# Optimization experiments

Measured on AMD Instinct MI355X. Metric: run time of the kernel, lower is better.

## Reference

```python
import jax, jax.numpy as jnp
import numpy as np

# ---- config mirrored from FullyFusedNGP.__init__ (scale=1) ----
SCALE = 1.0
L, F, LOG2_T, N_MIN = 16, 2, 19, 16
T = 1 << LOG2_T  # 524288 entries per level
B = float(np.exp(np.log(2048.0 * SCALE / N_MIN) / (L - 1)))  # per_level_scale
RES = np.array([int(np.ceil(N_MIN * B**l - 1.0)) + 1 for l in range(L)], dtype=np.int32)
PRIMES = np.array([1, 2654435761, 805459861], dtype=np.uint32)  # tcnn hash primes
CORNERS = np.array([[(i >> k) & 1 for k in range(3)] for i in range(8)], dtype=np.int32)  # [8,3]
N_PTS = 262144


def hash_encode(xn, table):
    """Multi-resolution hash grid with trilinear interpolation.
    xn: [N,3] in [0,1]; table: [L,T,F] -> returns [N, L*F]."""
    res = jnp.asarray(RES)
    corners = jnp.asarray(CORNERS)
    pos = xn[None] * (res[:, None, None] - 1).astype(xn.dtype)        # [L,N,3]
    p0 = jnp.floor(pos).astype(jnp.int32)
    w = pos - p0                                                      # [L,N,3] trilinear fracs
    idx = p0[:, :, None, :] + corners[None, None]                     # [L,N,8,3]
    idx = jnp.clip(idx, 0, (res - 1)[:, None, None, None])
    ui = idx.astype(jnp.uint32)
    h = (ui[..., 0] * PRIMES[0]) ^ (ui[..., 1] * PRIMES[1]) ^ (ui[..., 2] * PRIMES[2])
    h = (h & jnp.uint32(T - 1)).astype(jnp.int32)                     # [L,N,8]
    feats = jax.vmap(lambda t, hh: t[hh])(table, h)                   # [L,N,8,F] gather
    cw = jnp.where(corners[None, None].astype(bool),
                   w[:, :, None, :], 1.0 - w[:, :, None, :]).prod(-1)  # [L,N,8]
    feat = (feats * cw[..., None]).sum(2)                             # [L,N,F]
    return jnp.moveaxis(feat, 0, 1).reshape(xn.shape[0], L * F)       # [N,32]


def sh_encode(d01):
    """Spherical harmonics degree 4 (tcnn convention, input in [0,1]). [N,3]->[N,16]."""
    d = 2.0 * d01 - 1.0
    x, y, z = d[:, 0], d[:, 1], d[:, 2]
    xy, xz, yz = x * y, x * z, y * z
    x2, y2, z2 = x * x, y * y, z * z
    return jnp.stack([
        jnp.full_like(x, 0.28209479177387814),
        -0.48860251190291987 * y,
        0.48860251190291987 * z,
        -0.48860251190291987 * x,
        1.0925484305920792 * xy,
        -1.0925484305920792 * yz,
        0.94617469575755997 * z2 - 0.31539156525251999,
        -1.0925484305920792 * xz,
        0.54627421529603959 * (x2 - y2),
        0.59004358992664352 * y * (-3.0 * x2 + y2),
        2.8906114426405538 * xy * z,
        0.45704579946446572 * y * (1.0 - 5.0 * z2),
        0.3731763325901154 * z * (5.0 * z2 - 3.0),
        0.45704579946446572 * x * (1.0 - 5.0 * z2),
        1.4453057213202769 * z * (x2 - y2),
        0.59004358992664352 * x * (-x2 + 3.0 * y2),
    ], axis=1)


def setup_inputs() -> dict:
    key = jax.random.key(0)
    ks = jax.random.split(key, 8)
    x = jax.random.uniform(ks[0], (N_PTS, 3), jnp.float32, -SCALE, SCALE)
    d = jax.random.normal(ks[1], (N_PTS, 3), jnp.float32)
    d = d / jnp.linalg.norm(d, axis=1, keepdims=True)
    table = jax.random.uniform(ks[2], (L, T, F), jnp.float32, -1e-4, 1e-4)
    def w(k, fi, fo):  # bias-free FullyFusedMLP weights
        return jax.random.normal(k, (fi, fo), jnp.float32) * (1.0 / np.sqrt(fi))
    return {
        'x': x, 'd': d, 'table': table,
        'w1': w(ks[3], 32, 64), 'w2': w(ks[4], 64, 16),
        'w_in': w(ks[5], 32, 64), 'w_h': w(ks[6], 64, 64), 'w_out': w(ks[7], 64, 3),
    }


def reference(x, d, table, w1, w2, w_in, w_h, w_out):
    xn = (x + SCALE) / (2.0 * SCALE)                 # (x - xyz_min)/(xyz_max - xyz_min)
    enc = hash_encode(xn, table)                     # [N,32]
    h = jax.nn.relu(enc @ w1) @ w2                   # density MLP, 1 hidden layer -> [N,16]
    sigmas = jnp.exp(h[:, 0])                        # TruncExp forward == exp
    sh = sh_encode((d + 1.0) * 0.5)                  # [N,16]
    a = jax.nn.relu(jnp.concatenate([sh, h], axis=1) @ w_in)
    a = jax.nn.relu(a @ w_h)
    rgbs = jax.nn.sigmoid(a @ w_out)                 # [N,3]
    return sigmas, rgbs
```

## Files before the change

### kernel.cpp

```cpp
#include <hip/hip_runtime.h>
#include <hip/hip_bf16.h>
#include <stdint.h>

typedef __bf16 bf16x8 __attribute__((ext_vector_type(8)));
typedef float  f32x4  __attribute__((ext_vector_type(4)));

__device__ __forceinline__ int imin(int a, int b) { return a < b ? a : b; }
__device__ __forceinline__ int imax(int a, int b) { return a > b ? a : b; }

#define TMASK ((1u << 19) - 1u)

__constant__ int cRES[16] = {16, 23, 31, 43, 59, 81, 112, 154,
                             213, 295, 407, 562, 777, 1073, 1483, 2048};

__global__ void __launch_bounds__(256) ngp_encode2(
    const float* __restrict__ xin,
    const float2* __restrict__ tab,
    float2* __restrict__ enc,
    int n, int nblk_half)
{
    const int bid = blockIdx.x;
    const int half = (bid >= nblk_half) ? 1 : 0;
    const int b = bid - half * nblk_half;
    const int l = (b & 7) + 8 * half;
    const int pbase = (b >> 3) * 512 + threadIdx.x;

    const int rm = cRES[l] - 1;
    const float rf = (float)rm;
    const uint32_t base = (uint32_t)l << 19;

    uint32_t idx[2][8];
    float wa[2][3];

    #pragma unroll
    for (int q = 0; q < 2; ++q) {
        const int p = pbase + q * 256;
        const float xn0 = (xin[3 * p + 0] + 1.0f) * 0.5f;
        const float xn1 = (xin[3 * p + 1] + 1.0f) * 0.5f;
        const float xn2 = (xin[3 * p + 2] + 1.0f) * 0.5f;

        const float p0 = xn0 * rf, p1 = xn1 * rf, p2 = xn2 * rf;
        const float f0 = floorf(p0), f1 = floorf(p1), f2 = floorf(p2);
        const int i0 = (int)f0, i1 = (int)f1, i2 = (int)f2;
        wa[q][0] = p0 - f0; wa[q][1] = p1 - f1; wa[q][2] = p2 - f2;

        const int a0 = imax(imin(i0, rm), 0), b0 = imax(imin(i0 + 1, rm), 0);
        const int a1 = imax(imin(i1, rm), 0), b1 = imax(imin(i1 + 1, rm), 0);
        const int a2 = imax(imin(i2, rm), 0), b2 = imax(imin(i2 + 1, rm), 0);

        const uint32_t t0a = (uint32_t)a0;
        const uint32_t t0b = (uint32_t)b0;
        const uint32_t t1a = (uint32_t)a1 * 2654435761u;
        const uint32_t t1b = (uint32_t)b1 * 2654435761u;
        const uint32_t t2a = (uint32_t)a2 * 805459861u;
        const uint32_t t2b = (uint32_t)b2 * 805459861u;

        idx[q][0] = base + ((t0a ^ t1a ^ t2a) & TMASK);
        idx[q][1] = base + ((t0b ^ t1a ^ t2a) & TMASK);
        idx[q][2] = base + ((t0a ^ t1b ^ t2a) & TMASK);
        idx[q][3] = base + ((t0b ^ t1b ^ t2a) & TMASK);
        idx[q][4] = base + ((t0a ^ t1a ^ t2b) & TMASK);
        idx[q][5] = base + ((t0b ^ t1a ^ t2b) & TMASK);
        idx[q][6] = base + ((t0a ^ t1b ^ t2b) & TMASK);
        idx[q][7] = base + ((t0b ^ t1b ^ t2b) & TMASK);
    }

    float2 v[2][8];
    #pragma unroll
    for (int q = 0; q < 2; ++q)
        #pragma unroll
        for (int cor = 0; cor < 8; ++cor)
            v[q][cor] = tab[idx[q][cor]];

    __builtin_amdgcn_sched_barrier(0);

    #pragma unroll
    for (int q = 0; q < 2; ++q) {
        const float w0 = wa[q][0], w1 = wa[q][1], w2 = wa[q][2];
        const float u0 = 1.0f - w0, u1 = 1.0f - w1, u2 = 1.0f - w2;
        float e0 = 0.0f, e1 = 0.0f;
        {   float cw = u0 * u1 * u2;  e0 = fmaf(v[q][0].x, cw, e0); e1 = fmaf(v[q][0].y, cw, e1); }
        {   float cw = w0 * u1 * u2;  e0 = fmaf(v[q][1].x, cw, e0); e1 = fmaf(v[q][1].y, cw, e1); }
        {   float cw = u0 * w1 * u2;  e0 = fmaf(v[q][2].x, cw, e0); e1 = fmaf(v[q][2].y, cw, e1); }
        {   float cw = w0 * w1 * u2;  e0 = fmaf(v[q][3].x, cw, e0); e1 = fmaf(v[q][3].y, cw, e1); }
        {   float cw = u0 * u1 * w2;  e0 = fmaf(v[q][4].x, cw, e0); e1 = fmaf(v[q][4].y, cw, e1); }
        {   float cw = w0 * u1 * w2;  e0 = fmaf(v[q][5].x, cw, e0); e1 = fmaf(v[q][5].y, cw, e1); }
        {   float cw = u0 * w1 * w2;  e0 = fmaf(v[q][6].x, cw, e0); e1 = fmaf(v[q][6].y, cw, e1); }
        {   float cw = w0 * w1 * w2;  e0 = fmaf(v[q][7].x, cw, e0); e1 = fmaf(v[q][7].y, cw, e1); }

        union { double d; float2 f; } u;
        u.f = make_float2(e0, e1);
        const int p = pbase + q * 256;
        __builtin_nontemporal_store(u.d, (double*)&enc[(size_t)l * n + p]);
    }
}

__global__ void __launch_bounds__(256) ngp_mlp_mfma(
    const float2* __restrict__ enc,
    const float* __restrict__ din,
    const float* __restrict__ W1,
    const float* __restrict__ W2,
    const float* __restrict__ WIN,
    const float* __restrict__ WH,
    const float* __restrict__ WOUT,
    float* __restrict__ out,
    int n, int ntiles)
{
    __shared__ float lds[4][16 * 68];
    const int tid  = threadIdx.x;
    const int wid  = tid >> 6;
    const int lane = tid & 63;
    const int c = lane & 15;
    const int g = lane >> 4;
    float* buf = &lds[wid][0];

    bf16x8 w1f[4], w2f[2], winf[4], whf[2][4], woutf[2];
    #pragma unroll
    for (int n4 = 0; n4 < 4; ++n4)
        #pragma unroll
        for (int j = 0; j < 8; ++j)
            w1f[n4][j] = (__bf16)W1[(g * 8 + j) * 64 + n4 * 16 + c];
    #pragma unroll
    for (int kc = 0; kc < 2; ++kc)
        #pragma unroll
        for (int j = 0; j < 8; ++j)
            w2f[kc][j] = (__bf16)W2[(kc * 32 + g * 8 + j) * 16 + c];
    #pragma unroll
    for (int n4 = 0; n4 < 4; ++n4)
        #pragma unroll
        for (int j = 0; j < 8; ++j)
            winf[n4][j] = (__bf16)WIN[(g * 8 + j) * 64 + n4 * 16 + c];
    #pragma unroll
    for (int kc = 0; kc < 2; ++kc)
        #pragma unroll
        for (int n4 = 0; n4 < 4; ++n4)
            #pragma unroll
            for (int j = 0; j < 8; ++j)
                whf[kc][n4][j] = (__bf16)WH[(kc * 32 + g * 8 + j) * 64 + n4 * 16 + c];
    #pragma unroll
    for (int kc = 0; kc < 2; ++kc)
        #pragma unroll
        for (int j = 0; j < 8; ++j)
            woutf[kc][j] = (c < 3) ? (__bf16)WOUT[(kc * 32 + g * 8 + j) * 3 + c]
                                   : (__bf16)0.0f;

    for (int t = blockIdx.x; t < ntiles; t += gridDim.x) {
        const int pbase = t * 64 + wid * 16;
        const int pc = pbase + c;

        bf16x8 a1;
        #pragma unroll
        for (int m = 0; m < 4; ++m) {
            const float2 e = enc[(size_t)(4 * g + m) * n + pc];
            a1[2 * m]     = (__bf16)e.x;
            a1[2 * m + 1] = (__bf16)e.y;
        }

        #pragma unroll
        for (int n4 = 0; n4 < 4; ++n4) {
            f32x4 d = {0.f, 0.f, 0.f, 0.f};
            d = __builtin_amdgcn_mfma_f32_16x16x32_bf16(a1, w1f[n4], d, 0, 0, 0);
            #pragma unroll
            for (int r = 0; r < 4; ++r)
                buf[(g * 4 + r) * 68 + n4 * 16 + c] = fmaxf(d[r], 0.0f);
        }

        f32x4 hacc = {0.f, 0.f, 0.f, 0.f};
        #pragma unroll
        for (int kc = 0; kc < 2; ++kc) {
            bf16x8 a2;
            const float* src = &buf[c * 68 + kc * 32 + g * 8];
            #pragma unroll
            for (int j = 0; j < 8; ++j) a2[j] = (__bf16)src[j];
            hacc = __builtin_amdgcn_mfma_f32_16x16x32_bf16(a2, w2f[kc], hacc, 0, 0, 0);
        }

        if (c == 0) {
            #pragma unroll
            for (int r = 0; r < 4; ++r)
                out[pbase + g * 4 + r] = __expf(hacc[r]);
        }

        #pragma unroll
        for (int r = 0; r < 4; ++r)
            buf[(g * 4 + r) * 68 + c] = hacc[r];

        const float dx = din[3 * pc + 0];
        const float dy = din[3 * pc + 1];
        const float dz = din[3 * pc + 2];
        const float xy = dx * dy, xz = dx * dz, yz = dy * dz;
        const float x2 = dx * dx, y2 = dy * dy, z2 = dz * dz;
        float shv[16];
        shv[0]  = 0.28209479177387814f;
        shv[1]  = -0.48860251190291987f * dy;
        shv[2]  = 0.48860251190291987f * dz;
        shv[3]  = -0.48860251190291987f * dx;
        shv[4]  = 1.0925484305920792f * xy;
        shv[5]  = -1.0925484305920792f * yz;
        shv[6]  = 0.94617469575756f * z2 - 0.31539156525252f;
        shv[7]  = -1.0925484305920792f * xz;
        shv[8]  = 0.5462742152960396f * (x2 - y2);
        shv[9]  = 0.5900435899266435f * dy * (-3.0f * x2 + y2);
        shv[10] = 2.890611442640554f * xy * dz;
        shv[11] = 0.4570457994644657f * dy * (1.0f - 5.0f * z2);
        shv[12] = 0.3731763325901154f * dz * (5.0f * z2 - 3.0f);
        shv[13] = 0.4570457994644657f * dx * (1.0f - 5.0f * z2);
        shv[14] = 1.445305721320277f * dz * (x2 - y2);
        shv[15] = 0.5900435899266435f * dx * (-x2 + 3.0f * y2);

        bf16x8 a3;
        if (g < 2) {
            #pragma unroll
            for (int j = 0; j < 8; ++j) a3[j] = (__bf16)shv[g * 8 + j];
        } else {
            const float* hsrc = &buf[c * 68 + (g - 2) * 8];
            #pragma unroll
            for (int j = 0; j < 8; ++j) a3[j] = (__bf16)hsrc[j];
        }

        #pragma unroll
        for (int n4 = 0; n4 < 4; ++n4) {
            f32x4 d = {0.f, 0.f, 0.f, 0.f};
            d = __builtin_amdgcn_mfma_f32_16x16x32_bf16(a3, winf[n4], d, 0, 0, 0);
            #pragma unroll
            for (int r = 0; r < 4; ++r)
                buf[(g * 4 + r) * 68 + n4 * 16 + c] = fmaxf(d[r], 0.0f);
        }

        bf16x8 a4[2];
        #pragma unroll
        for (int kc = 0; kc < 2; ++kc) {
            const float* src = &buf[c * 68 + kc * 32 + g * 8];
            #pragma unroll
            for (int j = 0; j < 8; ++j) a4[kc][j] = (__bf16)src[j];
        }
        f32x4 d4[4];
        #pragma unroll
        for (int n4 = 0; n4 < 4; ++n4) d4[n4] = (f32x4){0.f, 0.f, 0.f, 0.f};
        #pragma unroll
        for (int kc = 0; kc < 2; ++kc)
            #pragma unroll
            for (int n4 = 0; n4 < 4; ++n4)
                d4[n4] = __builtin_amdgcn_mfma_f32_16x16x32_bf16(a4[kc], whf[kc][n4], d4[n4], 0, 0, 0);
        #pragma unroll
        for (int n4 = 0; n4 < 4; ++n4)
            #pragma unroll
            for (int r = 0; r < 4; ++r)
                buf[(g * 4 + r) * 68 + n4 * 16 + c] = fmaxf(d4[n4][r], 0.0f);

        f32x4 d5 = {0.f, 0.f, 0.f, 0.f};
        #pragma unroll
        for (int kc = 0; kc < 2; ++kc) {
            bf16x8 a5;
            const float* src = &buf[c * 68 + kc * 32 + g * 8];
            #pragma unroll
            for (int j = 0; j < 8; ++j) a5[j] = (__bf16)src[j];
            d5 = __builtin_amdgcn_mfma_f32_16x16x32_bf16(a5, woutf[kc], d5, 0, 0, 0);
        }
        if (c < 3) {
            #pragma unroll
            for (int r = 0; r < 4; ++r)
                out[n + 3 * (pbase + g * 4 + r) + c] = 1.0f / (1.0f + __expf(-d5[r]));
        }
    }
}

__global__ void __launch_bounds__(256) ngp_mlp(
    const float2* __restrict__ enc, const float* __restrict__ din,
    const float* __restrict__ W1, const float* __restrict__ W2,
    const float* __restrict__ WIN, const float* __restrict__ WH,
    const float* __restrict__ WOUT, float* __restrict__ out, int n)
{
    const int i = blockIdx.x * 256 + threadIdx.x;
    if (i >= n) return;
    float h1[64];
    #pragma unroll
    for (int j = 0; j < 64; ++j) h1[j] = 0.0f;
    #pragma unroll
    for (int l = 0; l < 16; ++l) {
        const float2 e = enc[(size_t)l * n + i];
        #pragma unroll
        for (int j = 0; j < 64; ++j)
            h1[j] = fmaf(e.x, W1[(2 * l) * 64 + j], fmaf(e.y, W1[(2 * l + 1) * 64 + j], h1[j]));
    }
    float h[16];
    #pragma unroll
    for (int j = 0; j < 16; ++j) h[j] = 0.0f;
    #pragma unroll
    for (int k = 0; k < 64; ++k) {
        const float v = fmaxf(h1[k], 0.0f);
        #pragma unroll
        for (int j = 0; j < 16; ++j) h[j] = fmaf(v, W2[k * 16 + j], h[j]);
    }
    out[i] = __expf(h[0]);
    const float dx = din[3 * i + 0], dy = din[3 * i + 1], dz = din[3 * i + 2];
    const float xy = dx * dy, xz = dx * dz, yz = dy * dz;
    const float x2 = dx * dx, y2 = dy * dy, z2 = dz * dz;
    float sh[16];
    sh[0]  = 0.28209479177387814f;
    sh[1]  = -0.48860251190291987f * dy;
    sh[2]  = 0.48860251190291987f * dz;
    sh[3]  = -0.48860251190291987f * dx;
    sh[4]  = 1.0925484305920792f * xy;
    sh[5]  = -1.0925484305920792f * yz;
    sh[6]  = 0.94617469575756f * z2 - 0.31539156525252f;
    sh[7]  = -1.0925484305920792f * xz;
    sh[8]  = 0.5462742152960396f * (x2 - y2);
    sh[9]  = 0.5900435899266435f * dy * (-3.0f * x2 + y2);
    sh[10] = 2.890611442640554f * xy * dz;
    sh[11] = 0.4570457994644657f * dy * (1.0f - 5.0f * z2);
    sh[12] = 0.3731763325901154f * dz * (5.0f * z2 - 3.0f);
    sh[13] = 0.4570457994644657f * dx * (1.0f - 5.0f * z2);
    sh[14] = 1.445305721320277f * dz * (x2 - y2);
    sh[15] = 0.5900435899266435f * dx * (-x2 + 3.0f * y2);
    float av[64];
    #pragma unroll
    for (int j = 0; j < 64; ++j) av[j] = 0.0f;
    #pragma unroll
    for (int k = 0; k < 16; ++k) {
        const float v = sh[k];
        #pragma unroll
        for (int j = 0; j < 64; ++j) av[j] = fmaf(v, WIN[k * 64 + j], av[j]);
    }
    #pragma unroll
    for (int k = 0; k < 16; ++k) {
        const float v = h[k];
        #pragma unroll
        for (int j = 0; j < 64; ++j) av[j] = fmaf(v, WIN[(16 + k) * 64 + j], av[j]);
    }
    float bv[64];
    #pragma unroll
    for (int j = 0; j < 64; ++j) bv[j] = 0.0f;
    #pragma unroll
    for (int k = 0; k < 64; ++k) {
        const float v = fmaxf(av[k], 0.0f);
        #pragma unroll
        for (int j = 0; j < 64; ++j) bv[j] = fmaf(v, WH[k * 64 + j], bv[j]);
    }
    float r0 = 0.0f, r1 = 0.0f, r2 = 0.0f;
    #pragma unroll
    for (int k = 0; k < 64; ++k) {
        const float v = fmaxf(bv[k], 0.0f);
        r0 = fmaf(v, WOUT[k * 3 + 0], r0);
        r1 = fmaf(v, WOUT[k * 3 + 1], r1);
        r2 = fmaf(v, WOUT[k * 3 + 2], r2);
    }
    out[n + 3 * i + 0] = 1.0f / (1.0f + __expf(-r0));
    out[n + 3 * i + 1] = 1.0f / (1.0f + __expf(-r1));
    out[n + 3 * i + 2] = 1.0f / (1.0f + __expf(-r2));
}

extern "C" void kernel_launch(void* const* d_in, const int* in_sizes, int n_in,
                              void* d_out, int out_size, void* d_ws, size_t ws_size,
                              hipStream_t stream)
{
    const float* x    = (const float*)d_in[0];
    const float* d    = (const float*)d_in[1];
    const float* tb   = (const float*)d_in[2];
    const float* w1   = (const float*)d_in[3];
    const float* w2   = (const float*)d_in[4];
    const float* win  = (const float*)d_in[5];
    const float* wh   = (const float*)d_in[6];
    const float* wout = (const float*)d_in[7];

    const int n = in_sizes[0] / 3;
    const size_t enc_bytes = (size_t)16 * n * sizeof(float2);
    float2* enc = (float2*)d_ws;

    const int nblk_half = (n / 512) * 8;
    ngp_encode2<<<2 * nblk_half, 256, 0, stream>>>(x, (const float2*)tb, enc, n, nblk_half);

    if (ws_size >= enc_bytes) {
        const int ntiles = n / 64;
        ngp_mlp_mfma<<<1024, 256, 0, stream>>>(enc, d, w1, w2, win, wh, wout,
                                               (float*)d_out, n, ntiles);
    } else {
        ngp_mlp<<<n / 256, 256, 0, stream>>>(enc, d, w1, w2, win, wh, wout,
                                             (float*)d_out, n);
    }
}
```

Measured before the change: 232.0 us.

## Fuse hash encode and MFMA MLP into one cooperative kernel with grid sync

Merges the encode and MLP kernels into a single cooperative launch of 1024 blocks. Each block first encodes its slice of points for two levels, mapping levels to XCDs by block index, then does a grid-wide sync and runs the MFMA MLP on a fixed set of four tiles. This removes one kernel launch and the gap between the two launches, at the cost of a grid barrier and lower encode parallelism, since each block now loops over 4x2 point groups. The scalar fallback MLP is dropped, and the fixed tile mapping hardcodes n=262144.

```diff
diff --git a/kernel.cpp b/kernel.cpp
--- a/kernel.cpp
+++ b/kernel.cpp
@@ -1,6 +1,9 @@
 #include <hip/hip_runtime.h>
 #include <hip/hip_bf16.h>
+#include <hip/hip_cooperative_groups.h>
 #include <stdint.h>
+
+namespace cg = cooperative_groups;
 
 typedef __bf16 bf16x8 __attribute__((ext_vector_type(8)));
 typedef float  f32x4  __attribute__((ext_vector_type(4)));
@@ -13,28 +16,16 @@
 __constant__ int cRES[16] = {16, 23, 31, 43, 59, 81, 112, 154,
                              213, 295, 407, 562, 777, 1073, 1483, 2048};
 
-__global__ void __launch_bounds__(256) ngp_encode2(
-    const float* __restrict__ xin,
-    const float2* __restrict__ tab,
-    float2* __restrict__ enc,
-    int n, int nblk_half)
+__device__ __forceinline__ void encode_pair(
+    const float* __restrict__ xin, const float2* __restrict__ tab,
+    float2* __restrict__ enc, int n, int l, int rm, float rf,
+    uint32_t base, int pb)
 {
-    const int bid = blockIdx.x;
-    const int half = (bid >= nblk_half) ? 1 : 0;
-    const int b = bid - half * nblk_half;
-    const int l = (b & 7) + 8 * half;
-    const int pbase = (b >> 3) * 512 + threadIdx.x;
-
-    const int rm = cRES[l] - 1;
-    const float rf = (float)rm;
-    const uint32_t base = (uint32_t)l << 19;
-
     uint32_t idx[2][8];
     float wa[2][3];
-
     #pragma unroll
     for (int q = 0; q < 2; ++q) {
-        const int p = pbase + q * 256;
+        const int p = pb + q * 256;
         const float xn0 = (xin[3 * p + 0] + 1.0f) * 0.5f;
         const float xn1 = (xin[3 * p + 1] + 1.0f) * 0.5f;
         const float xn2 = (xin[3 * p + 2] + 1.0f) * 0.5f;
@@ -90,21 +81,23 @@
 
         union { double d; float2 f; } u;
         u.f = make_float2(e0, e1);
-        const int p = pbase + q * 256;
+        const int p = pb + q * 256;
         __builtin_nontemporal_store(u.d, (double*)&enc[(size_t)l * n + p]);
     }
 }
 
-__global__ void __launch_bounds__(256) ngp_mlp_mfma(
-    const float2* __restrict__ enc,
+__global__ void __launch_bounds__(256, 4) ngp_coop(
+    const float* __restrict__ xin,
     const float* __restrict__ din,
+    const float2* __restrict__ tab,
     const float* __restrict__ W1,
     const float* __restrict__ W2,
     const float* __restrict__ WIN,
     const float* __restrict__ WH,
     const float* __restrict__ WOUT,
+    float2* __restrict__ enc,
     float* __restrict__ out,
-    int n, int ntiles)
+    int n)
 {
     __shared__ float lds[4][16 * 68];
     const int tid  = threadIdx.x;
@@ -114,6 +107,24 @@
     const int g = lane >> 4;
     float* buf = &lds[wid][0];
 
+    {
+        const int xcd  = blockIdx.x & 7;
+        const int brow = blockIdx.x >> 3;
+        #pragma unroll
+        for (int h = 0; h < 2; ++h) {
+            const int l = xcd + 8 * h;
+            const int rm = cRES[l] - 1;
+            const float rf = (float)rm;
+            const uint32_t base = (uint32_t)l << 19;
+            for (int it = 0; it < 4; ++it) {
+                const int pb = brow * 2048 + it * 512 + tid;
+                encode_pair(xin, tab, enc, n, l, rm, rf, base, pb);
+            }
+        }
+    }
+
+    cg::this_grid().sync();
+
     bf16x8 w1f[4], w2f[2], winf[4], whf[2][4], woutf[2];
     #pragma unroll
     for (int n4 = 0; n4 < 4; ++n4)
@@ -144,7 +155,8 @@
             woutf[kc][j] = (c < 3) ? (__bf16)WOUT[(kc * 32 + g * 8 + j) * 3 + c]
                                    : (__bf16)0.0f;
 
-    for (int t = blockIdx.x; t < ntiles; t += gridDim.x) {
+    for (int k = 0; k < 4; ++k) {
+        const int t = (blockIdx.x << 2) + k;
         const int pbase = t * 64 + wid * 16;
         const int pc = pbase + c;
 
@@ -265,89 +277,183 @@
     }
 }
 
-__global__ void __launch_bounds__(256) ngp_mlp(
+__global__ void __launch_bounds__(256) ngp_encode2(
+    const float* __restrict__ xin, const float2* __restrict__ tab,
+    float2* __restrict__ enc, int n, int nblk_half)
+{
+    const int bid = blockIdx.x;
+    const int half = (bid >= nblk_half) ? 1 : 0;
+    const int b = bid - half * nblk_half;
+    const int l = (b & 7) + 8 * half;
+    const int pbase = (b >> 3) * 512 + threadIdx.x;
+    const int rm = cRES[l] - 1;
+    encode_pair(xin, tab, enc, n, l, rm, (float)rm, (uint32_t)l << 19, pbase);
+}
+
+__global__ void __launch_bounds__(256) ngp_mlp_mfma(
     const float2* __restrict__ enc, const float* __restrict__ din,
     const float* __restrict__ W1, const float* __restrict__ W2,
     const float* __restrict__ WIN, const float* __restrict__ WH,
-    const float* __restrict__ WOUT, float* __restrict__ out, int n)
+    const float* __restrict__ WOUT, float* __restrict__ out,
+    int n, int ntiles)
 {
-    const int i = blockIdx.x * 256 + threadIdx.x;
-    if (i >= n) return;
-    float h1[64];
-    #pragma unroll
-    for (int j = 0; j < 64; ++j) h1[j] = 0.0f;
-    #pragma unroll
-    for (int l = 0; l < 16; ++l) {
-        const float2 e = enc[(size_t)l * n + i];
-        #pragma unroll
-        for (int j = 0; j < 64; ++j)
-            h1[j] = fmaf(e.x, W1[(2 * l) * 64 + j], fmaf(e.y, W1[(2 * l + 1) * 64 + j], h1[j]));
-    }
-    float h[16];
-    #pragma unroll
-    for (int j = 0; j < 16; ++j) h[j] = 0.0f;
-    #pragma unroll
-    for (int k = 0; k < 64; ++k) {
-        const float v = fmaxf(h1[k], 0.0f);
-        #pragma unroll
-        for (int j = 0; j < 16; ++j) h[j] = fmaf(v, W2[k * 16 + j], h[j]);
-    }
-    out[i] = __expf(h[0]);
-    const float dx = din[3 * i + 0], dy = din[3 * i + 1], dz = din[3 * i + 2];
-    const float xy = dx * dy, xz = dx * dz, yz = dy * dz;
-    const float x2 = dx * dx, y2 = dy * dy, z2 = dz * dz;
-    float sh[16];
-    sh[0]  = 0.28209479177387814f;
-    sh[1]  = -0.48860251190291987f * dy;
-    sh[2]  = 0.48860251190291987f * dz;
-    sh[3]  = -0.48860251190291987f * dx;
-    sh[4]  = 1.0925484305920792f * xy;
-    sh[5]  = -1.0925484305920792f * yz;
-    sh[6]  = 0.94617469575756f * z2 - 0.31539156525252f;
-    sh[7]  = -1.0925484305920792f * xz;
-    sh[8]  = 0.5462742152960396f * (x2 - y2);
-    sh[9]  = 0.5900435899266435f * dy * (-3.0f * x2 + y2);
-    sh[10] = 2.890611442640554f * xy * dz;
-    sh[11] = 0.4570457994644657f * dy * (1.0f - 5.0f * z2);
-    sh[12] = 0.3731763325901154f * dz * (5.0f * z2 - 3.0f);
-    sh[13] = 0.4570457994644657f * dx * (1.0f - 5.0f * z2);
-    sh[14] = 1.445305721320277f * dz * (x2 - y2);
-    sh[15] = 0.5900435899266435f * dx * (-x2 + 3.0f * y2);
-    float av[64];
-    #pragma unroll
-    for (int j = 0; j < 64; ++j) av[j] = 0.0f;
-    #pragma unroll
-    for (int k = 0; k < 16; ++k) {
-        const float v = sh[k];
-        #pragma unroll
-        for (int j = 0; j < 64; ++j) av[j] = fmaf(v, WIN[k * 64 + j], av[j]);
-    }
-    #pragma unroll
-    for (int k = 0; k < 16; ++k) {
-        const float v = h[k];
-        #pragma unroll
-        for (int j = 0; j < 64; ++j) av[j] = fmaf(v, WIN[(16 + k) * 64 + j], av[j]);
-    }
-    float bv[64];
-    #pragma unroll
-    for (int j = 0; j < 64; ++j) bv[j] = 0.0f;
-    #pragma unroll
-    for (int k = 0; k < 64; ++k) {
-        const float v = fmaxf(av[k], 0.0f);
-        #pragma unroll
-        for (int j = 0; j < 64; ++j) bv[j] = fmaf(v, WH[k * 64 + j], bv[j]);
-    }
-    float r0 = 0.0f, r1 = 0.0f, r2 = 0.0f;
-    #pragma unroll
-    for (int k = 0; k < 64; ++k) {
-        const float v = fmaxf(bv[k], 0.0f);
-        r0 = fmaf(v, WOUT[k * 3 + 0], r0);
-        r1 = fmaf(v, WOUT[k * 3 + 1], r1);
-        r2 = fmaf(v, WOUT[k * 3 + 2], r2);
-    }
-    out[n + 3 * i + 0] = 1.0f / (1.0f + __expf(-r0));
-    out[n + 3 * i + 1] = 1.0f / (1.0f + __expf(-r1));
-    out[n + 3 * i + 2] = 1.0f / (1.0f + __expf(-r2));
+    __shared__ float lds[4][16 * 68];
+    const int tid  = threadIdx.x;
+    const int wid  = tid >> 6;
+    const int lane = tid & 63;
+    const int c = lane & 15;
+    const int g = lane >> 4;
+    float* buf = &lds[wid][0];
+
+    bf16x8 w1f[4], w2f[2], winf[4], whf[2][4], woutf[2];
+    #pragma unroll
+    for (int n4 = 0; n4 < 4; ++n4)
+        #pragma unroll
+        for (int j = 0; j < 8; ++j)
+            w1f[n4][j] = (__bf16)W1[(g * 8 + j) * 64 + n4 * 16 + c];
+    #pragma unroll
+    for (int kc = 0; kc < 2; ++kc)
+        #pragma unroll
+        for (int j = 0; j < 8; ++j)
+            w2f[kc][j] = (__bf16)W2[(kc * 32 + g * 8 + j) * 16 + c];
+    #pragma unroll
+    for (int n4 = 0; n4 < 4; ++n4)
+        #pragma unroll
+        for (int j = 0; j < 8; ++j)
+            winf[n4][j] = (__bf16)WIN[(g * 8 + j) * 64 + n4 * 16 + c];
+    #pragma unroll
+    for (int kc = 0; kc < 2; ++kc)
+        #pragma unroll
+        for (int n4 = 0; n4 < 4; ++n4)
+            #pragma unroll
+            for (int j = 0; j < 8; ++j)
+                whf[kc][n4][j] = (__bf16)WH[(kc * 32 + g * 8 + j) * 64 + n4 * 16 + c];
+    #pragma unroll
+    for (int kc = 0; kc < 2; ++kc)
+        #pragma unroll
+        for (int j = 0; j < 8; ++j)
+            woutf[kc][j] = (c < 3) ? (__bf16)WOUT[(kc * 32 + g * 8 + j) * 3 + c]
+                                   : (__bf16)0.0f;
+
+    for (int t = blockIdx.x; t < ntiles; t += gridDim.x) {
+        const int pbase = t * 64 + wid * 16;
+        const int pc = pbase + c;
+
+        bf16x8 a1;
+        #pragma unroll
+        for (int m = 0; m < 4; ++m) {
+            const float2 e = enc[(size_t)(4 * g + m) * n + pc];
+            a1[2 * m]     = (__bf16)e.x;
+            a1[2 * m + 1] = (__bf16)e.y;
+        }
+
+        #pragma unroll
+        for (int n4 = 0; n4 < 4; ++n4) {
+            f32x4 d = {0.f, 0.f, 0.f, 0.f};
+            d = __builtin_amdgcn_mfma_f32_16x16x32_bf16(a1, w1f[n4], d, 0, 0, 0);
+            #pragma unroll
+            for (int r = 0; r < 4; ++r)
+                buf[(g * 4 + r) * 68 + n4 * 16 + c] = fmaxf(d[r], 0.0f);
+        }
+
+        f32x4 hacc = {0.f, 0.f, 0.f, 0.f};
+        #pragma unroll
+        for (int kc = 0; kc < 2; ++kc) {
+            bf16x8 a2;
+            const float* src = &buf[c * 68 + kc * 32 + g * 8];
+            #pragma unroll
+            for (int j = 0; j < 8; ++j) a2[j] = (__bf16)src[j];
+            hacc = __builtin_amdgcn_mfma_f32_16x16x32_bf16(a2, w2f[kc], hacc, 0, 0, 0);
+        }
+
+        if (c == 0) {
+            #pragma unroll
+            for (int r = 0; r < 4; ++r)
+                out[pbase + g * 4 + r] = __expf(hacc[r]);
+        }
+
+        #pragma unroll
+        for (int r = 0; r < 4; ++r)
+            buf[(g * 4 + r) * 68 + c] = hacc[r];
+
+        const float dx = din[3 * pc + 0];
+        const float dy = din[3 * pc + 1];
+        const float dz = din[3 * pc + 2];
+        const float xy = dx * dy, xz = dx * dz, yz = dy * dz;
+        const float x2 = dx * dx, y2 = dy * dy, z2 = dz * dz;
+        float shv[16];
+        shv[0]  = 0.28209479177387814f;
+        shv[1]  = -0.48860251190291987f * dy;
+        shv[2]  = 0.48860251190291987f * dz;
+        shv[3]  = -0.48860251190291987f * dx;
+        shv[4]  = 1.0925484305920792f * xy;
+        shv[5]  = -1.0925484305920792f * yz;
+        shv[6]  = 0.94617469575756f * z2 - 0.31539156525252f;
+        shv[7]  = -1.0925484305920792f * xz;
+        shv[8]  = 0.5462742152960396f * (x2 - y2);
+        shv[9]  = 0.5900435899266435f * dy * (-3.0f * x2 + y2);
+        shv[10] = 2.890611442640554f * xy * dz;
+        shv[11] = 0.4570457994644657f * dy * (1.0f - 5.0f * z2);
+        shv[12] = 0.3731763325901154f * dz * (5.0f * z2 - 3.0f);
+        shv[13] = 0.4570457994644657f * dx * (1.0f - 5.0f * z2);
+        shv[14] = 1.445305721320277f * dz * (x2 - y2);
+        shv[15] = 0.5900435899266435f * dx * (-x2 + 3.0f * y2);
+
+        bf16x8 a3;
+        if (g < 2) {
+            #pragma unroll
+            for (int j = 0; j < 8; ++j) a3[j] = (__bf16)shv[g * 8 + j];
+        } else {
+            const float* hsrc = &buf[c * 68 + (g - 2) * 8];
+            #pragma unroll
+            for (int j = 0; j < 8; ++j) a3[j] = (__bf16)hsrc[j];
+        }
+
+        #pragma unroll
+        for (int n4 = 0; n4 < 4; ++n4) {
+            f32x4 d = {0.f, 0.f, 0.f, 0.f};
+            d = __builtin_amdgcn_mfma_f32_16x16x32_bf16(a3, winf[n4], d, 0, 0, 0);
+            #pragma unroll
+            for (int r = 0; r < 4; ++r)
+                buf[(g * 4 + r) * 68 + n4 * 16 + c] = fmaxf(d[r], 0.0f);
+        }
+
+        bf16x8 a4[2];
+        #pragma unroll
+        for (int kc = 0; kc < 2; ++kc) {
+            const float* src = &buf[c * 68 + kc * 32 + g * 8];
+            #pragma unroll
+            for (int j = 0; j < 8; ++j) a4[kc][j] = (__bf16)src[j];
+        }
+        f32x4 d4[4];
+        #pragma unroll
+        for (int n4 = 0; n4 < 4; ++n4) d4[n4] = (f32x4){0.f, 0.f, 0.f, 0.f};
+        #pragma unroll
+        for (int kc = 0; kc < 2; ++kc)
+            #pragma unroll
+            for (int n4 = 0; n4 < 4; ++n4)
+                d4[n4] = __builtin_amdgcn_mfma_f32_16x16x32_bf16(a4[kc], whf[kc][n4], d4[n4], 0, 0, 0);
+        #pragma unroll
+        for (int n4 = 0; n4 < 4; ++n4)
+            #pragma unroll
+            for (int r = 0; r < 4; ++r)
+                buf[(g * 4 + r) * 68 + n4 * 16 + c] = fmaxf(d4[n4][r], 0.0f);
+
+        f32x4 d5 = {0.f, 0.f, 0.f, 0.f};
+        #pragma unroll
+        for (int kc = 0; kc < 2; ++kc) {
+            bf16x8 a5;
+            const float* src = &buf[c * 68 + kc * 32 + g * 8];
+            #pragma unroll
+            for (int j = 0; j < 8; ++j) a5[j] = (__bf16)src[j];
+            d5 = __builtin_amdgcn_mfma_f32_16x16x32_bf16(a5, woutf[kc], d5, 0, 0, 0);
+        }
+        if (c < 3) {
+            #pragma unroll
+            for (int r = 0; r < 4; ++r)
+                out[n + 3 * (pbase + g * 4 + r) + c] = 1.0f / (1.0f + __expf(-d5[r]));
+        }
+    }
 }
 
 extern "C" void kernel_launch(void* const* d_in, const int* in_sizes, int n_in,
@@ -363,19 +469,22 @@
     const float* wh   = (const float*)d_in[6];
     const float* wout = (const float*)d_in[7];
 
-    const int n = in_sizes[0] / 3;
-    const size_t enc_bytes = (size_t)16 * n * sizeof(float2);
+    int n = in_sizes[0] / 3;
     float2* enc = (float2*)d_ws;
-
-    const int nblk_half = (n / 512) * 8;
-    ngp_encode2<<<2 * nblk_half, 256, 0, stream>>>(x, (const float2*)tb, enc, n, nblk_half);
-
-    if (ws_size >= enc_bytes) {
-        const int ntiles = n / 64;
+    float* outp = (float*)d_out;
+    const float2* tab = (const float2*)tb;
+
+    void* args[] = { (void*)&x, (void*)&d, (void*)&tab,
+                     (void*)&w1, (void*)&w2, (void*)&win, (void*)&wh, (void*)&wout,
+                     (void*)&enc, (void*)&outp, (void*)&n };
+
+    hipError_t e = hipLaunchCooperativeKernel((const void*)ngp_coop,
+                                              dim3(1024), dim3(256),
+                                              args, 0, stream);
+    if (e != hipSuccess) {
+        const int nblk_half = (n / 512) * 8;
+        ngp_encode2<<<2 * nblk_half, 256, 0, stream>>>(x, tab, enc, n, nblk_half);
         ngp_mlp_mfma<<<1024, 256, 0, stream>>>(enc, d, w1, w2, win, wh, wout,
-                                               (float*)d_out, n, ntiles);
-    } else {
-        ngp_mlp<<<n / 256, 256, 0, stream>>>(enc, d, w1, w2, win, wh, wout,
-                                             (float*)d_out, n);
+                                               outp, n, 4096);
     }
 }
```

Result: slower. 438.0 us (+88.8%).
